# Performance work log

Hardware: AMD Instinct MI355X
Metric: run time of the kernel (lower is better)

## Reference

```python
import jax, jax.numpy as jnp
import numpy as np

N_NODES = 50000
N_EDGES = 640000
NFEAT = 128
NHID = 128
BN_EPS = 1e-5
GIN_EPS = 0.0  # GINConv default eps


def setup_inputs() -> dict:
    key = jax.random.key(0)
    ks = jax.random.split(key, 8)
    x = jax.random.normal(ks[0], (N_NODES, NFEAT), dtype=jnp.float32)
    edge_index = jax.random.randint(ks[1], (2, N_EDGES), 0, N_NODES, dtype=jnp.int64)
    # xavier-uniform linears, zero bias (per weights_init); BN gamma=1, beta=0
    def xavier(k, fan_in, fan_out):
        a = float(np.sqrt(6.0 / (fan_in + fan_out)))
        return jax.random.uniform(k, (fan_in, fan_out), dtype=jnp.float32, minval=-a, maxval=a)
    W1 = xavier(ks[2], NFEAT, NHID)
    b1 = jnp.zeros((NHID,), dtype=jnp.float32)
    gamma = jnp.ones((NHID,), dtype=jnp.float32)
    beta = jnp.zeros((NHID,), dtype=jnp.float32)
    W2 = xavier(ks[3], NHID, NHID)
    b2 = jnp.zeros((NHID,), dtype=jnp.float32)
    return {"x": x, "edge_index": edge_index, "W1": W1, "b1": b1,
            "gamma": gamma, "beta": beta, "W2": W2, "b2": b2}


def reference(x, edge_index, W1, b1, gamma, beta, W2, b2):
    src, dst = edge_index[0], edge_index[1]
    # sparse neighbor sum-aggregation: agg[i] = sum_{(src->dst=i)} x[src]
    agg = jax.ops.segment_sum(x[src], dst, num_segments=x.shape[0])
    h = (1.0 + GIN_EPS) * x + agg
    # MLP: Linear -> ReLU -> BatchNorm1d (training-mode batch stats) -> Linear
    h = jax.nn.relu(h @ W1 + b1)
    mean = jnp.mean(h, axis=0)
    var = jnp.mean(jnp.square(h - mean), axis=0)  # biased var, as torch BN uses
    h = (h - mean) * jax.lax.rsqrt(var + BN_EPS) * gamma + beta
    return h @ W2 + b2
```

## Files before the change

### kernel.cpp

```cpp
#include <hip/hip_runtime.h>
#include <hip/hip_fp16.h>

#define NNODES 50000
#define NEDGES 640000
#define NF 128
#define XB 3125
#define WB 64
#define BINS 196
#define BINCAP 4096
#define P1AB 313
#define EPB 2048

typedef __attribute__((ext_vector_type(8))) _Float16 f16x8;
typedef __attribute__((ext_vector_type(4))) float f32x4;

__global__ __launch_bounds__(256) void k_prep(const float* __restrict__ x,
                                              const float* __restrict__ W1,
                                              const int* __restrict__ ei,
                                              unsigned short* __restrict__ xh,
                                              _Float16* __restrict__ wp1,
                                              int* __restrict__ cnt,
                                              float* __restrict__ stats) {
  __shared__ int lcnt[BINS];
  const int bid = blockIdx.x, t = threadIdx.x;
  if (bid < XB) {
    int i = bid * 256 + t;
    const float4 a = ((const float4*)x)[2 * i];
    const float4 b = ((const float4*)x)[2 * i + 1];
    __half2 h0 = __float22half2_rn(make_float2(a.x, a.y));
    __half2 h1 = __float22half2_rn(make_float2(a.z, a.w));
    __half2 h2 = __float22half2_rn(make_float2(b.x, b.y));
    __half2 h3 = __float22half2_rn(make_float2(b.z, b.w));
    uint4 v;
    v.x = *(unsigned*)&h0; v.y = *(unsigned*)&h1;
    v.z = *(unsigned*)&h2; v.w = *(unsigned*)&h3;
    ((uint4*)xh)[i] = v;
    if (bid == 0) { stats[t] = 0.f; stats[256 + t] = 0.f; }
  } else if (bid < XB + WB) {
    int f = (bid - XB) * 256 + t;
    int j = f & 7, lane = (f >> 3) & 63, cf = (f >> 9) & 7, ks = f >> 12;
    int k = ks * 32 + ((lane >> 4) << 3) + j;
    int n = cf * 16 + (lane & 15);
    float w = W1[k * NF + n];
    _Float16 hi = (_Float16)w;
    _Float16 lo = (_Float16)(w - (float)hi);
    wp1[f] = hi;
    wp1[16384 + f] = lo;
  } else {
    const int blk = bid - (XB + WB);
    const int e0 = blk * EPB;
    const bool full = (e0 + EPB <= NEDGES);
    if (t < BINS) lcnt[t] = 0;
    __syncthreads();
    const int4 d0 = *(const int4*)(ei + NEDGES + e0 + 4 * t);
    atomicAdd(&lcnt[d0.x >> 8], 1);
    atomicAdd(&lcnt[d0.y >> 8], 1);
    atomicAdd(&lcnt[d0.z >> 8], 1);
    atomicAdd(&lcnt[d0.w >> 8], 1);
    if (full) {
      const int4 d1 = *(const int4*)(ei + NEDGES + e0 + 1024 + 4 * t);
      atomicAdd(&lcnt[d1.x >> 8], 1);
      atomicAdd(&lcnt[d1.y >> 8], 1);
      atomicAdd(&lcnt[d1.z >> 8], 1);
      atomicAdd(&lcnt[d1.w >> 8], 1);
    }
    __syncthreads();
    if (t < BINS) cnt[blk * BINS + t] = lcnt[t];
  }
}

__global__ __launch_bounds__(512) void k_p1b(const int* __restrict__ cnt,
                                             int* __restrict__ base,
                                             int* __restrict__ gtot) {
  __shared__ int s[512];
  const int t = threadIdx.x, b = blockIdx.x;
  const int v = (t < P1AB) ? cnt[t * BINS + b] : 0;
  s[t] = v;
  __syncthreads();
  for (int d = 1; d < 512; d <<= 1) {
    int u = (t >= d) ? s[t - d] : 0;
    __syncthreads();
    s[t] += u;
    __syncthreads();
  }
  if (t < P1AB) base[t * BINS + b] = s[t] - v;
  if (t == 511) gtot[b] = s[511];
}

__global__ __launch_bounds__(256) void k_p1c(const int* __restrict__ ei,
                                             const int* __restrict__ base,
                                             unsigned* __restrict__ binbuf) {
  __shared__ int lcur[BINS];
  const int t = threadIdx.x, blk = blockIdx.x;
  const int e0 = blk * EPB;
  const bool full = (e0 + EPB <= NEDGES);
  if (t < BINS) lcur[t] = base[blk * BINS + t];
  __syncthreads();
  const int4 s0 = *(const int4*)(ei + e0 + 4 * t);
  const int4 d0 = *(const int4*)(ei + NEDGES + e0 + 4 * t);
#define SCAT(ss, dd)                                                             \
  {                                                                              \
    int bin = (dd) >> 8;                                                         \
    int pos = atomicAdd(&lcur[bin], 1);                                          \
    if (pos < BINCAP)                                                            \
      binbuf[bin * BINCAP + pos] = ((unsigned)((dd) & 255) << 16) | (unsigned)(ss); \
  }
  SCAT(s0.x, d0.x); SCAT(s0.y, d0.y); SCAT(s0.z, d0.z); SCAT(s0.w, d0.w);
  if (full) {
    const int4 s1 = *(const int4*)(ei + e0 + 1024 + 4 * t);
    const int4 d1 = *(const int4*)(ei + NEDGES + e0 + 1024 + 4 * t);
    SCAT(s1.x, d1.x); SCAT(s1.y, d1.y); SCAT(s1.z, d1.z); SCAT(s1.w, d1.w);
  }
#undef SCAT
}

__global__ __launch_bounds__(256) void k_p2(const unsigned* __restrict__ binbuf,
                                            const int* __restrict__ gtot,
                                            int* __restrict__ begdeg,
                                            unsigned short* __restrict__ slot) {
  __shared__ int cnt2[256], pst[256];
  __shared__ unsigned short stg[BINCAP];
  const int t = threadIdx.x;
  const int b = blockIdx.x;
  const int base = b * BINCAP;
  const int nb = min(gtot[b], BINCAP);
  unsigned pk[16];
#pragma unroll
  for (int ci = 0; ci < 16; ++ci) {
    int i = (ci << 8) + t;
    pk[ci] = (i < nb) ? binbuf[base + i] : 0xFFFFFFFFu;
  }
  cnt2[t] = 0;
  __syncthreads();
#pragma unroll
  for (int ci = 0; ci < 16; ++ci)
    if (pk[ci] != 0xFFFFFFFFu) atomicAdd(&cnt2[(int)(pk[ci] >> 16)], 1);
  __syncthreads();
  pst[t] = cnt2[t];
  __syncthreads();
  for (int d = 1; d < 256; d <<= 1) {
    int u = (t >= d) ? pst[t - d] : 0;
    __syncthreads();
    pst[t] += u;
    __syncthreads();
  }
  pst[t] -= cnt2[t];
  int node = (b << 8) + t;
  if (node < NNODES)
    begdeg[node] = ((base + pst[t]) << 8) | min(cnt2[t], 255);
  cnt2[t] = 0;
  __syncthreads();
#pragma unroll
  for (int ci = 0; ci < 16; ++ci)
    if (pk[ci] != 0xFFFFFFFFu) {
      int dl = (int)(pk[ci] >> 16);
      int pos = atomicAdd(&cnt2[dl], 1);
      stg[pst[dl] + pos] = (unsigned short)(pk[ci] & 0xffffu);
    }
  __syncthreads();
  for (int i = t; i < nb; i += 256) slot[base + i] = stg[i];
}

__device__ inline void add8h(float* a, uint4 v) {
  const __half2* p = (const __half2*)&v;
#pragma unroll
  for (int q = 0; q < 4; ++q) {
    float2 f = __half22float2(p[q]);
    a[2 * q] += f.x;
    a[2 * q + 1] += f.y;
  }
}

__global__ __launch_bounds__(256) void k_gather(const unsigned short* __restrict__ xh,
                                                const int* __restrict__ begdeg,
                                                const unsigned short* __restrict__ slot,
                                                _Float16* __restrict__ h) {
  const int t = threadIdx.x;
  const int wv = t >> 6, l = t & 63;
  const int node = blockIdx.x * 4 + wv;
  if (node >= NNODES) return;
  const int cg = (l & 15) << 3;
  const int e = l >> 4;
  const int bd = begdeg[node];
  const int beg = bd >> 8;
  const int end = beg + (bd & 255);
  float a[8] = {0.f, 0.f, 0.f, 0.f, 0.f, 0.f, 0.f, 0.f};
  float b[8] = {0.f, 0.f, 0.f, 0.f, 0.f, 0.f, 0.f, 0.f};
  int j = beg + e;
  for (; j + 4 < end; j += 8) {
    const uint4 v0 = *(const uint4*)(xh + (size_t)slot[j] * NF + cg);
    const uint4 v1 = *(const uint4*)(xh + (size_t)slot[j + 4] * NF + cg);
    add8h(a, v0);
    add8h(b, v1);
  }
  if (j < end) {
    const uint4 v0 = *(const uint4*)(xh + (size_t)slot[j] * NF + cg);
    add8h(a, v0);
  }
#pragma unroll
  for (int q = 0; q < 8; ++q) a[q] += b[q];
#pragma unroll
  for (int q = 0; q < 8; ++q) {
    a[q] += __shfl_xor(a[q], 16);
    a[q] += __shfl_xor(a[q], 32);
  }
  if (e == 0) {
    const uint4 sv = *(const uint4*)(xh + (size_t)node * NF + cg);
    add8h(a, sv);
    f16x8 o;
#pragma unroll
    for (int q = 0; q < 8; ++q) o[q] = (_Float16)a[q];
    *(f16x8*)(h + (size_t)node * NF + cg) = o;
  }
}

template <int MODE>
__global__ __launch_bounds__(256, 2) void k_gemm(const _Float16* __restrict__ A,
                                                 const _Float16* __restrict__ wprep,
                                                 const float* __restrict__ bias,
                                                 float* __restrict__ stats,
                                                 _Float16* __restrict__ outh,
                                                 float* __restrict__ outf) {
  __shared__ _Float16 wl[32768];
  __shared__ float red[2][4][128];

  const int t = threadIdx.x;
  const int wv = t >> 6;
  const int l = t & 63;
  const int wrow0 = blockIdx.x * 128 + wv * 16;

  f16x8 areg[2][4];
#pragma unroll
  for (int m = 0; m < 2; ++m) {
    const int arow = wrow0 + m * 64 + (l & 15);
    const bool okA = arow < NNODES;
#pragma unroll
    for (int ks = 0; ks < 4; ++ks) {
      if (okA) {
        areg[m][ks] = *(const f16x8*)(A + (size_t)arow * NF + ks * 32 + ((l >> 4) << 3));
      } else {
        areg[m][ks] = (f16x8){};
      }
    }
  }

  const float4* src = (const float4*)wprep;
#pragma unroll
  for (int it = 0; it < 16; ++it) {
    ((float4*)wl)[it * 256 + t] = src[it * 256 + t];
  }
  __syncthreads();

  f32x4 acc[2][8];
#pragma unroll
  for (int m = 0; m < 2; ++m)
#pragma unroll
    for (int cf = 0; cf < 8; ++cf) acc[m][cf] = (f32x4){0.f, 0.f, 0.f, 0.f};

#pragma unroll
  for (int ks = 0; ks < 4; ++ks) {
#pragma unroll
    for (int cf = 0; cf < 8; ++cf) {
      const int fo = (((ks * 8 + cf) << 6) + l) << 3;
      f16x8 bh = *(const f16x8*)(wl + fo);
      f16x8 bl = *(const f16x8*)(wl + 16384 + fo);
#pragma unroll
      for (int m = 0; m < 2; ++m) {
        acc[m][cf] = __builtin_amdgcn_mfma_f32_16x16x32_f16(areg[m][ks], bh, acc[m][cf], 0, 0, 0);
        acc[m][cf] = __builtin_amdgcn_mfma_f32_16x16x32_f16(areg[m][ks], bl, acc[m][cf], 0, 0, 0);
      }
    }
  }

  const int col16 = l & 15;
  const int rg = l >> 4;
  float bl_[8];
#pragma unroll
  for (int cf = 0; cf < 8; ++cf) bl_[cf] = bias[cf * 16 + col16];

  if (MODE == 0) {
    float cs[8], cq[8];
#pragma unroll
    for (int cf = 0; cf < 8; ++cf) { cs[cf] = 0.f; cq[cf] = 0.f; }
#pragma unroll
    for (int m = 0; m < 2; ++m)
#pragma unroll
      for (int cf = 0; cf < 8; ++cf) {
#pragma unroll
        for (int r = 0; r < 4; ++r) {
          int row = wrow0 + m * 64 + rg * 4 + r;
          if (row < NNODES) {
            float v = fmaxf(acc[m][cf][r] + bl_[cf], 0.f);
            outh[(size_t)row * NF + cf * 16 + col16] = (_Float16)v;
            cs[cf] += v;
            cq[cf] += v * v;
          }
        }
      }
#pragma unroll
    for (int cf = 0; cf < 8; ++cf) {
      cs[cf] += __shfl_xor(cs[cf], 16); cs[cf] += __shfl_xor(cs[cf], 32);
      cq[cf] += __shfl_xor(cq[cf], 16); cq[cf] += __shfl_xor(cq[cf], 32);
    }
    if (l < 16) {
#pragma unroll
      for (int cf = 0; cf < 8; ++cf) {
        red[0][wv][cf * 16 + l] = cs[cf];
        red[1][wv][cf * 16 + l] = cq[cf];
      }
    }
    __syncthreads();
    if (t < 128) {
      float s = red[0][0][t] + red[0][1][t] + red[0][2][t] + red[0][3][t];
      float q = red[1][0][t] + red[1][1][t] + red[1][2][t] + red[1][3][t];
      unsafeAtomicAdd(stats + t, s);
      unsafeAtomicAdd(stats + 128 + t, q);
    }
  } else {
#pragma unroll
    for (int m = 0; m < 2; ++m)
#pragma unroll
      for (int cf = 0; cf < 8; ++cf) {
#pragma unroll
        for (int r = 0; r < 4; ++r) {
          int row = wrow0 + m * 64 + rg * 4 + r;
          if (row < NNODES)
            outf[(size_t)row * NF + cf * 16 + col16] = acc[m][cf][r] + bl_[cf];
        }
      }
  }
}

__global__ __launch_bounds__(256) void k_fold(const float* __restrict__ stats,
                                              const float* __restrict__ gamma,
                                              const float* __restrict__ beta,
                                              const float* __restrict__ W2,
                                              const float* __restrict__ b2,
                                              _Float16* __restrict__ wp2,
                                              float* __restrict__ b2p) {
  __shared__ float sc_s[128], sh_s[128];
  __shared__ float part[2][128];
  const int t = threadIdx.x, bb = blockIdx.x;
  if (t < 128) {
    const float inv = 1.0f / (float)NNODES;
    float mean = stats[t] * inv;
    float var = stats[128 + t] * inv - mean * mean;
    var = fmaxf(var, 0.f);
    float sc = gamma[t] * rsqrtf(var + 1e-5f);
    sc_s[t] = sc;
    sh_s[t] = beta[t] - mean * sc;
  }
  __syncthreads();
  if (bb < 16) {
#pragma unroll
    for (int it = 0; it < 4; ++it) {
      int f = bb * 1024 + it * 256 + t;
      int j = f & 7, lane = (f >> 3) & 63, cf = (f >> 9) & 7, ks = f >> 12;
      int k = ks * 32 + ((lane >> 4) << 3) + j;
      int n = cf * 16 + (lane & 15);
      float w = sc_s[k] * W2[k * NF + n];
      _Float16 hi = (_Float16)w;
      _Float16 lo = (_Float16)(w - (float)hi);
      wp2[f] = hi;
      wp2[16384 + f] = lo;
    }
  } else {
    const int col = t & 127, ch = t >> 7;
    float s = 0.f;
    for (int k = ch * 64; k < ch * 64 + 64; ++k) s += sh_s[k] * W2[k * NF + col];
    part[ch][col] = s;
    __syncthreads();
    if (t < 128) b2p[t] = b2[t] + part[0][t] + part[1][t];
  }
}

extern "C" void kernel_launch(void* const* d_in, const int* in_sizes, int n_in,
                              void* d_out, int out_size, void* d_ws, size_t ws_size,
                              hipStream_t stream) {
  const float* x     = (const float*)d_in[0];
  const int*   ei    = (const int*)d_in[1];
  const float* W1    = (const float*)d_in[2];
  const float* b1    = (const float*)d_in[3];
  const float* gamma = (const float*)d_in[4];
  const float* beta  = (const float*)d_in[5];
  const float* W2    = (const float*)d_in[6];
  const float* b2    = (const float*)d_in[7];
  float* out = (float*)d_out;

  _Float16* h = (_Float16*)d_out;

  float*          stats  = (float*)d_ws;
  _Float16*       wp1    = (_Float16*)(stats + 512);
  _Float16*       wp2    = wp1 + 32768;
  float*          b2p    = (float*)(wp2 + 32768);
  int*            cnt    = (int*)(b2p + 128);
  int*            basep  = cnt + 61376;
  int*            gtot   = basep + 61376;
  int*            begdeg = gtot + 256;
  unsigned*       binbuf = (unsigned*)(begdeg + 50176);
  unsigned short* slot   = (unsigned short*)(binbuf + BINS * BINCAP);
  unsigned short* xh     = slot + BINS * BINCAP;
  _Float16*       h1     = (_Float16*)(xh + (size_t)NNODES * NF);

  k_prep   <<<XB + WB + P1AB, 256, 0, stream>>>(x, W1, ei, xh, wp1, cnt, stats);
  k_p1b    <<<BINS, 512, 0, stream>>>(cnt, basep, gtot);
  k_p1c    <<<P1AB, 256, 0, stream>>>(ei, basep, binbuf);
  k_p2     <<<BINS, 256, 0, stream>>>(binbuf, gtot, begdeg, slot);
  k_gather <<<(NNODES + 3) / 4, 256, 0, stream>>>(xh, begdeg, slot, h);
  k_gemm<0><<<(NNODES + 127) / 128, 256, 0, stream>>>(h, wp1, b1, stats, h1, nullptr);
  k_fold   <<<17, 256, 0, stream>>>(stats, gamma, beta, W2, b2, wp2, b2p);
  k_gemm<1><<<(NNODES + 127) / 128, 256, 0, stream>>>(h1, wp2, b2p, nullptr, nullptr, out);
}
```

Before: 90.56 us.

## Fuse weight prep and BN folding into GEMM kernels, drop k_fold launch

Each GEMM block now converts the fp32 weights into the split hi/lo fp16 MFMA layout in shared memory itself. The second GEMM also computes the BN scale and shift and the folded bias from the stats. This removes the k_fold kernel launch and the weight-prep blocks in k_prep, cutting one launch and a serialization point. In exchange, every one of the 391 blocks redundantly reads the 64KB fp32 weights with strided scalar loads and does the conversion and a 64-step bias dot product, adding prologue latency per block.

```diff
diff --git a/kernel.cpp b/kernel.cpp
--- a/kernel.cpp
+++ b/kernel.cpp
@@ -5,7 +5,6 @@
 #define NEDGES 640000
 #define NF 128
 #define XB 3125
-#define WB 64
 #define BINS 196
 #define BINCAP 4096
 #define P1AB 313
@@ -15,10 +14,8 @@
 typedef __attribute__((ext_vector_type(4))) float f32x4;
 
 __global__ __launch_bounds__(256) void k_prep(const float* __restrict__ x,
-                                              const float* __restrict__ W1,
                                               const int* __restrict__ ei,
                                               unsigned short* __restrict__ xh,
-                                              _Float16* __restrict__ wp1,
                                               int* __restrict__ cnt,
                                               float* __restrict__ stats) {
   __shared__ int lcnt[BINS];
@@ -36,18 +33,8 @@
     v.z = *(unsigned*)&h2; v.w = *(unsigned*)&h3;
     ((uint4*)xh)[i] = v;
     if (bid == 0) { stats[t] = 0.f; stats[256 + t] = 0.f; }
-  } else if (bid < XB + WB) {
-    int f = (bid - XB) * 256 + t;
-    int j = f & 7, lane = (f >> 3) & 63, cf = (f >> 9) & 7, ks = f >> 12;
-    int k = ks * 32 + ((lane >> 4) << 3) + j;
-    int n = cf * 16 + (lane & 15);
-    float w = W1[k * NF + n];
-    _Float16 hi = (_Float16)w;
-    _Float16 lo = (_Float16)(w - (float)hi);
-    wp1[f] = hi;
-    wp1[16384 + f] = lo;
   } else {
-    const int blk = bid - (XB + WB);
+    const int blk = bid - XB;
     const int e0 = blk * EPB;
     const bool full = (e0 + EPB <= NEDGES);
     if (t < BINS) lcnt[t] = 0;
@@ -179,7 +166,7 @@
   const int wv = t >> 6, l = t & 63;
   const int node = blockIdx.x * 4 + wv;
   if (node >= NNODES) return;
-  const int cg = (l & 15) << 3;
+  const int cg_ = (l & 15) << 3;
   const int e = l >> 4;
   const int bd = begdeg[node];
   const int beg = bd >> 8;
@@ -188,13 +175,13 @@
   float b[8] = {0.f, 0.f, 0.f, 0.f, 0.f, 0.f, 0.f, 0.f};
   int j = beg + e;
   for (; j + 4 < end; j += 8) {
-    const uint4 v0 = *(const uint4*)(xh + (size_t)slot[j] * NF + cg);
-    const uint4 v1 = *(const uint4*)(xh + (size_t)slot[j + 4] * NF + cg);
+    const uint4 v0 = *(const uint4*)(xh + (size_t)slot[j] * NF + cg_);
+    const uint4 v1 = *(const uint4*)(xh + (size_t)slot[j + 4] * NF + cg_);
     add8h(a, v0);
     add8h(b, v1);
   }
   if (j < end) {
-    const uint4 v0 = *(const uint4*)(xh + (size_t)slot[j] * NF + cg);
+    const uint4 v0 = *(const uint4*)(xh + (size_t)slot[j] * NF + cg_);
     add8h(a, v0);
   }
 #pragma unroll
@@ -205,24 +192,27 @@
     a[q] += __shfl_xor(a[q], 32);
   }
   if (e == 0) {
-    const uint4 sv = *(const uint4*)(xh + (size_t)node * NF + cg);
+    const uint4 sv = *(const uint4*)(xh + (size_t)node * NF + cg_);
     add8h(a, sv);
     f16x8 o;
 #pragma unroll
     for (int q = 0; q < 8; ++q) o[q] = (_Float16)a[q];
-    *(f16x8*)(h + (size_t)node * NF + cg) = o;
+    *(f16x8*)(h + (size_t)node * NF + cg_) = o;
   }
 }
 
 template <int MODE>
 __global__ __launch_bounds__(256, 2) void k_gemm(const _Float16* __restrict__ A,
-                                                 const _Float16* __restrict__ wprep,
+                                                 const float* __restrict__ W,
                                                  const float* __restrict__ bias,
+                                                 const float* __restrict__ gamma,
+                                                 const float* __restrict__ beta,
                                                  float* __restrict__ stats,
                                                  _Float16* __restrict__ outh,
                                                  float* __restrict__ outf) {
   __shared__ _Float16 wl[32768];
   __shared__ float red[2][4][128];
+  __shared__ float scs[128], shs[128], b2sh[128];
 
   const int t = threadIdx.x;
   const int wv = t >> 6;
@@ -244,12 +234,48 @@
     }
   }
 
-  const float4* src = (const float4*)wprep;
-#pragma unroll
-  for (int it = 0; it < 16; ++it) {
-    ((float4*)wl)[it * 256 + t] = src[it * 256 + t];
-  }
-  __syncthreads();
+  if (MODE == 1) {
+    if (t < 128) {
+      const float inv = 1.0f / (float)NNODES;
+      float mean = stats[t] * inv;
+      float var = fmaxf(stats[128 + t] * inv - mean * mean, 0.f);
+      float sc = gamma[t] * rsqrtf(var + 1e-5f);
+      scs[t] = sc;
+      shs[t] = beta[t] - mean * sc;
+    }
+    __syncthreads();
+  }
+
+#pragma unroll
+  for (int oct = 0; oct < 8; ++oct) {
+    int f8 = oct * 256 + t;
+    int ks = f8 >> 9, cf = (f8 >> 6) & 7, lane = f8 & 63;
+    int k0 = ks * 32 + ((lane >> 4) << 3);
+    int n = cf * 16 + (lane & 15);
+    f16x8 hi, lo;
+#pragma unroll
+    for (int j = 0; j < 8; ++j) {
+      float w = W[(k0 + j) * NF + n];
+      if (MODE == 1) w *= scs[k0 + j];
+      _Float16 h_ = (_Float16)w;
+      hi[j] = h_;
+      lo[j] = (_Float16)(w - (float)h_);
+    }
+    *(f16x8*)(wl + f8 * 8) = hi;
+    *(f16x8*)(wl + 16384 + f8 * 8) = lo;
+  }
+
+  if (MODE == 1) {
+    const int col = t & 127, half = t >> 7;
+    float s = 0.f;
+    for (int k = half * 64; k < half * 64 + 64; ++k) s += shs[k] * W[k * NF + col];
+    red[0][half][col] = s;
+  }
+  __syncthreads();
+  if (MODE == 1) {
+    if (t < 128) b2sh[t] = bias[t] + red[0][0][t] + red[0][1][t];
+    __syncthreads();
+  }
 
   f32x4 acc[2][8];
 #pragma unroll
@@ -276,7 +302,8 @@
   const int rg = l >> 4;
   float bl_[8];
 #pragma unroll
-  for (int cf = 0; cf < 8; ++cf) bl_[cf] = bias[cf * 16 + col16];
+  for (int cf = 0; cf < 8; ++cf)
+    bl_[cf] = (MODE == 0) ? bias[cf * 16 + col16] : b2sh[cf * 16 + col16];
 
   if (MODE == 0) {
     float cs[8], cq[8];
@@ -302,6 +329,7 @@
       cs[cf] += __shfl_xor(cs[cf], 16); cs[cf] += __shfl_xor(cs[cf], 32);
       cq[cf] += __shfl_xor(cq[cf], 16); cq[cf] += __shfl_xor(cq[cf], 32);
     }
+    __syncthreads();
     if (l < 16) {
 #pragma unroll
       for (int cf = 0; cf < 8; ++cf) {
@@ -328,49 +356,6 @@
             outf[(size_t)row * NF + cf * 16 + col16] = acc[m][cf][r] + bl_[cf];
         }
       }
-  }
-}
-
-__global__ __launch_bounds__(256) void k_fold(const float* __restrict__ stats,
-                                              const float* __restrict__ gamma,
-                                              const float* __restrict__ beta,
-                                              const float* __restrict__ W2,
-                                              const float* __restrict__ b2,
-                                              _Float16* __restrict__ wp2,
-                                              float* __restrict__ b2p) {
-  __shared__ float sc_s[128], sh_s[128];
-  __shared__ float part[2][128];
-  const int t = threadIdx.x, bb = blockIdx.x;
-  if (t < 128) {
-    const float inv = 1.0f / (float)NNODES;
-    float mean = stats[t] * inv;
-    float var = stats[128 + t] * inv - mean * mean;
-    var = fmaxf(var, 0.f);
-    float sc = gamma[t] * rsqrtf(var + 1e-5f);
-    sc_s[t] = sc;
-    sh_s[t] = beta[t] - mean * sc;
-  }
-  __syncthreads();
-  if (bb < 16) {
-#pragma unroll
-    for (int it = 0; it < 4; ++it) {
-      int f = bb * 1024 + it * 256 + t;
-      int j = f & 7, lane = (f >> 3) & 63, cf = (f >> 9) & 7, ks = f >> 12;
-      int k = ks * 32 + ((lane >> 4) << 3) + j;
-      int n = cf * 16 + (lane & 15);
-      float w = sc_s[k] * W2[k * NF + n];
-      _Float16 hi = (_Float16)w;
-      _Float16 lo = (_Float16)(w - (float)hi);
-      wp2[f] = hi;
-      wp2[16384 + f] = lo;
-    }
-  } else {
-    const int col = t & 127, ch = t >> 7;
-    float s = 0.f;
-    for (int k = ch * 64; k < ch * 64 + 64; ++k) s += sh_s[k] * W2[k * NF + col];
-    part[ch][col] = s;
-    __syncthreads();
-    if (t < 128) b2p[t] = b2[t] + part[0][t] + part[1][t];
   }
 }
 
@@ -390,10 +375,7 @@
   _Float16* h = (_Float16*)d_out;
 
   float*          stats  = (float*)d_ws;
-  _Float16*       wp1    = (_Float16*)(stats + 512);
-  _Float16*       wp2    = wp1 + 32768;
-  float*          b2p    = (float*)(wp2 + 32768);
-  int*            cnt    = (int*)(b2p + 128);
+  int*            cnt    = (int*)(stats + 512);
   int*            basep  = cnt + 61376;
   int*            gtot   = basep + 61376;
   int*            begdeg = gtot + 256;
@@ -402,12 +384,13 @@
   unsigned short* xh     = slot + BINS * BINCAP;
   _Float16*       h1     = (_Float16*)(xh + (size_t)NNODES * NF);
 
-  k_prep   <<<XB + WB + P1AB, 256, 0, stream>>>(x, W1, ei, xh, wp1, cnt, stats);
+  k_prep   <<<XB + P1AB, 256, 0, stream>>>(x, ei, xh, cnt, stats);
   k_p1b    <<<BINS, 512, 0, stream>>>(cnt, basep, gtot);
   k_p1c    <<<P1AB, 256, 0, stream>>>(ei, basep, binbuf);
   k_p2     <<<BINS, 256, 0, stream>>>(binbuf, gtot, begdeg, slot);
   k_gather <<<(NNODES + 3) / 4, 256, 0, stream>>>(xh, begdeg, slot, h);
-  k_gemm<0><<<(NNODES + 127) / 128, 256, 0, stream>>>(h, wp1, b1, stats, h1, nullptr);
-  k_fold   <<<17, 256, 0, stream>>>(stats, gamma, beta, W2, b2, wp2, b2p);
-  k_gemm<1><<<(NNODES + 127) / 128, 256, 0, stream>>>(h1, wp2, b2p, nullptr, nullptr, out);
-}
+  k_gemm<0><<<(NNODES + 127) / 128, 256, 0, stream>>>(h, W1, b1, nullptr, nullptr,
+                                                      stats, h1, nullptr);
+  k_gemm<1><<<(NNODES + 127) / 128, 256, 0, stream>>>(h1, W2, b2, gamma, beta,
+                                                      stats, nullptr, out);
+}
```

Measured after the change: 88.85 us. About the same (-1.9%).
